# Optimization experiments

Hardware: AMD Instinct MI355X
Metric: run time of the kernel (lower is better)

## Reference

```python
import jax, jax.numpy as jnp
import numpy as np

E = 1024  # embedding_dim
H = 64    # head_size

def setup_inputs() -> dict:
    key = jax.random.key(0)
    k1, k2, k3, k4 = jax.random.split(key, 4)
    x = jax.random.normal(k1, (4, 4096, E), dtype=jnp.float32)
    # nn.Linear(E, H, bias=False) weights have shape [H, E]; y = x @ W.T
    s = 1.0 / np.sqrt(E)
    Wq = jax.random.normal(k2, (H, E), dtype=jnp.float32) * s
    Wk = jax.random.normal(k3, (H, E), dtype=jnp.float32) * s
    Wv = jax.random.normal(k4, (H, E), dtype=jnp.float32) * s
    return {"x": x, "Wq": Wq, "Wk": Wk, "Wv": Wv}

def reference(x, Wq, Wk, Wv):
    B, T, E_ = x.shape
    q = jnp.einsum('bte,he->bth', x, Wq)
    k = jnp.einsum('bte,he->bth', x, Wk)
    v = jnp.einsum('bte,he->bth', x, Wv)
    # NOTE: original scales by sqrt(embedding_dim), not head_size
    scores = jnp.einsum('bqh,bkh->bqk', q, k) / jnp.sqrt(jnp.asarray(E_, x.dtype))
    causal = jnp.tril(jnp.ones((T, T), dtype=bool))
    scores = jnp.where(causal, scores, -jnp.inf)
    weights = jax.nn.softmax(scores, axis=-1)
    return jnp.einsum('bqk,bkh->bqh', weights, v)
```

## Files before the change

### kernel.cpp

```cpp
#include <hip/hip_runtime.h>
#include <stdint.h>

typedef __bf16 bf16x8 __attribute__((ext_vector_type(8)));
typedef float  f32x4  __attribute__((ext_vector_type(4)));

#define E_DIM 1024
#define H_DIM 64
#define T_SEQ 4096
#define B_BAT 4
#define M_TOT (B_BAT * T_SEQ)

__device__ __forceinline__ ushort f2bfu(float f) {
    return __builtin_bit_cast(ushort, (__bf16)f);
}
__device__ __forceinline__ uint32_t pk2(float lo, float hi) {
    return (uint32_t)f2bfu(lo) | ((uint32_t)f2bfu(hi) << 16);
}
__device__ __forceinline__ float ex2(float x) {
    return __builtin_amdgcn_exp2f(x);
}
__device__ __forceinline__ bf16x8 ldfrag(const ushort* p) {
    return __builtin_bit_cast(bf16x8, *(const uint4*)(p));
}
__device__ __forceinline__ void barrier_lgkm() {
    __builtin_amdgcn_s_waitcnt(0xC07F);
    __builtin_amdgcn_s_barrier();
}

__global__ __launch_bounds__(256) void wcvt(const float* __restrict__ Wq,
                                            const float* __restrict__ Wk,
                                            const float* __restrict__ Wv,
                                            ushort* __restrict__ Wfm) {
    int g = blockIdx.x * 256 + threadIdx.x;
    int n = g >> 7;
    int k8 = g & 127;
    const float* src = (n < 64) ? (Wq + (size_t)n * E_DIM)
                     : (n < 128) ? (Wk + (size_t)(n - 64) * E_DIM)
                     : (Wv + (size_t)(n - 128) * E_DIM);
    float sc = (n < 64) ? 0.045084220f : 1.0f;
    float4 a = *(const float4*)(src + k8 * 8);
    float4 b = *(const float4*)(src + k8 * 8 + 4);
    uint4 o;
    o.x = pk2(a.x * sc, a.y * sc); o.y = pk2(a.z * sc, a.w * sc);
    o.z = pk2(b.x * sc, b.y * sc); o.w = pk2(b.z * sc, b.w * sc);
    int s = k8 >> 3, kc = (k8 >> 2) & 1, qd = k8 & 3;
    int nt = n >> 4, lm = n & 15;
    int lane = qd * 16 + lm;
    *(uint4*)(Wfm + (((size_t)(s * 12 + nt) * 2 + kc) * 64 + lane) * 8) = o;
}

__global__ __launch_bounds__(256, 3) void qkv(const float* __restrict__ x,
                                              const ushort* __restrict__ Wfm,
                                              ushort* __restrict__ Qfm,
                                              ushort* __restrict__ Kfm,
                                              ushort* __restrict__ Vfm) {
    __shared__ union {
        ushort a[2][32 * 72];
        struct { ushort c[32 * 136]; ushort vt[64 * 40]; } epi;
    } sm;
    const int tid = threadIdx.x;
    const int w = tid >> 6, l = tid & 63;
    const int lm = l & 15, qd = l >> 4;
    const int m0 = blockIdx.x * 32;

    f32x4 acc[2][3];
#pragma unroll
    for (int r2 = 0; r2 < 2; ++r2)
#pragma unroll
        for (int t = 0; t < 3; ++t) acc[r2][t] = (f32x4){0.f, 0.f, 0.f, 0.f};

    const int srow = tid >> 3, kseg = tid & 7;
    const float* xsrc = x + (size_t)(m0 + srow) * E_DIM + kseg * 8;

    {
        float4 a0 = *(const float4*)xsrc;
        float4 a1 = *(const float4*)(xsrc + 4);
        uint4 u = {pk2(a0.x, a0.y), pk2(a0.z, a0.w), pk2(a1.x, a1.y), pk2(a1.z, a1.w)};
        *(uint4*)(&sm.a[0][srow * 72 + kseg * 8]) = u;
    }
    float4 xa0 = *(const float4*)(xsrc + 64);
    float4 xa1 = *(const float4*)(xsrc + 68);
    float4 xb0 = *(const float4*)(xsrc + 128);
    float4 xb1 = *(const float4*)(xsrc + 132);
    __syncthreads();

    for (int s = 0; s < 16; ++s) {
        const int cb = s & 1, nb = cb ^ 1;
        float4 xc0 = xa0, xc1 = xa1;
        if (s < 13) {
            xc0 = *(const float4*)(xsrc + (s + 3) * 64);
            xc1 = *(const float4*)(xsrc + (s + 3) * 64 + 4);
        }
        bf16x8 wf[3][2];
#pragma unroll
        for (int t = 0; t < 3; ++t)
#pragma unroll
            for (int kc = 0; kc < 2; ++kc)
                wf[t][kc] = ldfrag(Wfm + (((size_t)(s * 12 + w * 3 + t) * 2 + kc) * 64 + l) * 8);
        bf16x8 af[2][2];
#pragma unroll
        for (int r2 = 0; r2 < 2; ++r2)
#pragma unroll
            for (int kc = 0; kc < 2; ++kc)
                af[r2][kc] = ldfrag(&sm.a[cb][(r2 * 16 + lm) * 72 + kc * 32 + qd * 8]);
#pragma unroll
        for (int t = 0; t < 3; ++t)
#pragma unroll
            for (int kc = 0; kc < 2; ++kc)
#pragma unroll
                for (int r2 = 0; r2 < 2; ++r2)
                    acc[r2][t] = __builtin_amdgcn_mfma_f32_16x16x32_bf16(af[r2][kc], wf[t][kc], acc[r2][t], 0, 0, 0);
        if (s < 15) {
            uint4 u = {pk2(xa0.x, xa0.y), pk2(xa0.z, xa0.w), pk2(xa1.x, xa1.y), pk2(xa1.z, xa1.w)};
            *(uint4*)(&sm.a[nb][srow * 72 + kseg * 8]) = u;
        }
        xa0 = xb0; xa1 = xb1; xb0 = xc0; xb1 = xc1;
        if (s < 15) barrier_lgkm();
    }
    __syncthreads();

#pragma unroll
    for (int r2 = 0; r2 < 2; ++r2)
#pragma unroll
        for (int t = 0; t < 3; ++t) {
            int gc = w * 48 + t * 16 + lm;
            int m = r2 * 16 + qd * 4;
#pragma unroll
            for (int rr = 0; rr < 4; ++rr) {
                ushort v = f2bfu(acc[r2][t][rr]);
                if (gc < 128) sm.epi.c[(m + rr) * 136 + gc] = v;
                else          sm.epi.vt[(gc - 128) * 40 + (m + rr)] = v;
            }
        }
    __syncthreads();

    const int g16b = m0 >> 4;
    const int kt64 = m0 >> 6;
    const int tb   = (m0 >> 4) & 3;
    const int kcv  = (m0 >> 5) & 1;
#pragma unroll
    for (int ii = 0; ii < 3; ++ii) {
        int i = w + ii * 4;
        uint4 val;
        ushort* dst;
        if (i < 4) {
            int qt_l = i >> 1, kc = i & 1;
            val = *(const uint4*)(&sm.epi.c[(qt_l * 16 + lm) * 136 + kc * 32 + qd * 8]);
            dst = Qfm + (((size_t)(g16b + qt_l) * 2 + kc) * 64 + l) * 8;
        } else if (i < 8) {
            int j2 = i - 4, t_l = j2 >> 1, kc = j2 & 1;
            val = *(const uint4*)(&sm.epi.c[(t_l * 16 + lm) * 136 + 64 + kc * 32 + qd * 8]);
            dst = Kfm + (((size_t)((kt64 * 4 + tb + t_l) * 2 + kc)) * 64 + l) * 8;
        } else {
            int t = i - 8;
            val = *(const uint4*)(&sm.epi.vt[(t * 16 + lm) * 40 + qd * 8]);
            dst = Vfm + (((size_t)((kt64 * 4 + t) * 2 + kcv)) * 64 + l) * 8;
        }
        *(uint4*)dst = val;
    }
}

__global__ __launch_bounds__(256, 2) void flashm(const ushort* __restrict__ Qfm,
                                                 const ushort* __restrict__ Kfm,
                                                 const ushort* __restrict__ Vfm,
                                                 float* __restrict__ out) {
    __shared__ union {
        ushort plds[4][2][16 * 72];
        struct { float ro[4][16][68]; float rl[4][16]; } red;
    } sm;
    const int tid = threadIdx.x;
    const int wv = tid >> 6, l = tid & 63;
    const int lm = l & 15, qd = l >> 4;
    const int pr = blockIdx.x;
    const int bt = blockIdx.y;
    const int jA = pr, jB = 255 - pr;
    const int ktdA = jA >> 2, tdA = jA & 3;
    const int ktdB = jB >> 2, tdB = jB & 3;
    ushort* mypA = sm.plds[wv][0];
    ushort* mypB = sm.plds[wv][1];

    bf16x8 qA0, qA1, qB0, qB1;
    {
        const ushort* qp = Qfm + ((size_t)(bt * 256 + jA) * 2) * 512 + l * 8;
        qA0 = ldfrag(qp); qA1 = ldfrag(qp + 512);
        const ushort* qq = Qfm + ((size_t)(bt * 256 + jB) * 2) * 512 + l * 8;
        qB0 = ldfrag(qq); qB1 = ldfrag(qq + 512);
    }
    f32x4 oA[4], oB[4];
#pragma unroll
    for (int t = 0; t < 4; ++t) {
        oA[t] = (f32x4){0.f, 0.f, 0.f, 0.f};
        oB[t] = (f32x4){0.f, 0.f, 0.f, 0.f};
    }
    float laccA = 0.f, laccB = 0.f;

    auto emitP = [&](const f32x4* sf, ushort* wp, bool diag, int td, float& lacc) {
#pragma unroll
        for (int t = 0; t < 4; ++t) {
            if (!diag || t < td) {
                float p0 = ex2(sf[t][0]), p1 = ex2(sf[t][1]);
                float p2 = ex2(sf[t][2]), p3 = ex2(sf[t][3]);
                lacc += (p0 + p1) + (p2 + p3);
                *(uint2*)(wp + t * 16) = uint2{pk2(p0, p1), pk2(p2, p3)};
            } else if (t == td) {
                float p[4];
#pragma unroll
                for (int rr = 0; rr < 4; ++rr) {
                    float pe = ex2(sf[t][rr]);
                    if (qd * 4 + rr > lm) pe = 0.f;
                    lacc += pe;
                    p[rr] = pe;
                }
                *(uint2*)(wp + t * 16) = uint2{pk2(p[0], p[1]), pk2(p[2], p[3])};
            } else {
                *(uint2*)(wp + t * 16) = uint2{0u, 0u};
            }
        }
    };
    auto pv = [&](const ushort* myp, const uint4 (&vu)[4][2], f32x4* o) {
        bf16x8 p0 = ldfrag(myp + lm * 72 + qd * 8);
        bf16x8 p1 = ldfrag(myp + lm * 72 + 32 + qd * 8);
#pragma unroll
        for (int t = 0; t < 4; ++t) {
            bf16x8 v0 = __builtin_bit_cast(bf16x8, vu[t][0]);
            bf16x8 v1 = __builtin_bit_cast(bf16x8, vu[t][1]);
            o[t] = __builtin_amdgcn_mfma_f32_16x16x32_bf16(p0, v0, o[t], 0, 0, 0);
            o[t] = __builtin_amdgcn_mfma_f32_16x16x32_bf16(p1, v1, o[t], 0, 0, 0);
        }
    };

    int kt = wv;
#pragma unroll 1
    for (; kt <= ktdA; kt += 4) {
        const ushort* kb = Kfm + ((size_t)(bt * 64 + kt) * 8) * 512;
        const ushort* vb = Vfm + ((size_t)(bt * 64 + kt) * 8) * 512;
        f32x4 sfA[4], sfB[4];
#pragma unroll
        for (int t = 0; t < 4; ++t) {
            sfA[t] = (f32x4){0.f, 0.f, 0.f, 0.f};
            sfB[t] = (f32x4){0.f, 0.f, 0.f, 0.f};
        }
#pragma unroll
        for (int t = 0; t < 4; ++t) {
            bf16x8 k0 = ldfrag(kb + (t * 2 + 0) * 512 + l * 8);
            bf16x8 k1 = ldfrag(kb + (t * 2 + 1) * 512 + l * 8);
            sfB[t] = __builtin_amdgcn_mfma_f32_16x16x32_bf16(k0, qB0, sfB[t], 0, 0, 0);
            sfB[t] = __builtin_amdgcn_mfma_f32_16x16x32_bf16(k1, qB1, sfB[t], 0, 0, 0);
            sfA[t] = __builtin_amdgcn_mfma_f32_16x16x32_bf16(k0, qA0, sfA[t], 0, 0, 0);
            sfA[t] = __builtin_amdgcn_mfma_f32_16x16x32_bf16(k1, qA1, sfA[t], 0, 0, 0);
        }
        uint4 vu[4][2];
#pragma unroll
        for (int t = 0; t < 4; ++t) {
            vu[t][0] = *(const uint4*)(vb + (t * 2 + 0) * 512 + l * 8);
            vu[t][1] = *(const uint4*)(vb + (t * 2 + 1) * 512 + l * 8);
        }
        emitP(sfB, mypB + lm * 72 + qd * 4, false, tdB, laccB);
        emitP(sfA, mypA + lm * 72 + qd * 4, kt == ktdA, tdA, laccA);
        __builtin_amdgcn_wave_barrier();
        __builtin_amdgcn_s_waitcnt(0xC07F);
        __builtin_amdgcn_wave_barrier();
        pv(mypB, vu, oB);
        pv(mypA, vu, oA);
        __builtin_amdgcn_wave_barrier();
    }
#pragma unroll 1
    for (; kt <= ktdB; kt += 4) {
        const ushort* kb = Kfm + ((size_t)(bt * 64 + kt) * 8) * 512;
        const ushort* vb = Vfm + ((size_t)(bt * 64 + kt) * 8) * 512;
        f32x4 sfB[4];
#pragma unroll
        for (int t = 0; t < 4; ++t) sfB[t] = (f32x4){0.f, 0.f, 0.f, 0.f};
#pragma unroll
        for (int t = 0; t < 4; ++t) {
            bf16x8 k0 = ldfrag(kb + (t * 2 + 0) * 512 + l * 8);
            bf16x8 k1 = ldfrag(kb + (t * 2 + 1) * 512 + l * 8);
            sfB[t] = __builtin_amdgcn_mfma_f32_16x16x32_bf16(k0, qB0, sfB[t], 0, 0, 0);
            sfB[t] = __builtin_amdgcn_mfma_f32_16x16x32_bf16(k1, qB1, sfB[t], 0, 0, 0);
        }
        uint4 vu[4][2];
#pragma unroll
        for (int t = 0; t < 4; ++t) {
            vu[t][0] = *(const uint4*)(vb + (t * 2 + 0) * 512 + l * 8);
            vu[t][1] = *(const uint4*)(vb + (t * 2 + 1) * 512 + l * 8);
        }
        emitP(sfB, mypB + lm * 72 + qd * 4, kt == ktdB, tdB, laccB);
        __builtin_amdgcn_wave_barrier();
        __builtin_amdgcn_s_waitcnt(0xC07F);
        __builtin_amdgcn_wave_barrier();
        pv(mypB, vu, oB);
        __builtin_amdgcn_wave_barrier();
    }

    laccA += __shfl_xor(laccA, 16); laccA += __shfl_xor(laccA, 32);
    laccB += __shfl_xor(laccB, 16); laccB += __shfl_xor(laccB, 32);

    __syncthreads();
    if (qd == 0) sm.red.rl[wv][lm] = laccA;
#pragma unroll
    for (int t = 0; t < 4; ++t)
#pragma unroll
        for (int rr = 0; rr < 4; ++rr)
            sm.red.ro[wv][qd * 4 + rr][t * 16 + lm] = oA[t][rr];
    __syncthreads();
    {
        const int row = wv * 4 + qd;
        float ls = sm.red.rl[0][row] + sm.red.rl[1][row] + sm.red.rl[2][row] + sm.red.rl[3][row];
        float inv = 1.0f / ls;
        float4 s0 = *(const float4*)&sm.red.ro[0][row][lm * 4];
        float4 s1 = *(const float4*)&sm.red.ro[1][row][lm * 4];
        float4 s2 = *(const float4*)&sm.red.ro[2][row][lm * 4];
        float4 s3 = *(const float4*)&sm.red.ro[3][row][lm * 4];
        float4 ov;
        ov.x = (s0.x + s1.x + s2.x + s3.x) * inv;
        ov.y = (s0.y + s1.y + s2.y + s3.y) * inv;
        ov.z = (s0.z + s1.z + s2.z + s3.z) * inv;
        ov.w = (s0.w + s1.w + s2.w + s3.w) * inv;
        *(float4*)(out + ((size_t)bt * T_SEQ + jA * 16 + row) * 64 + lm * 4) = ov;
    }
    __syncthreads();
    if (qd == 0) sm.red.rl[wv][lm] = laccB;
#pragma unroll
    for (int t = 0; t < 4; ++t)
#pragma unroll
        for (int rr = 0; rr < 4; ++rr)
            sm.red.ro[wv][qd * 4 + rr][t * 16 + lm] = oB[t][rr];
    __syncthreads();
    {
        const int row = wv * 4 + qd;
        float ls = sm.red.rl[0][row] + sm.red.rl[1][row] + sm.red.rl[2][row] + sm.red.rl[3][row];
        float inv = 1.0f / ls;
        float4 s0 = *(const float4*)&sm.red.ro[0][row][lm * 4];
        float4 s1 = *(const float4*)&sm.red.ro[1][row][lm * 4];
        float4 s2 = *(const float4*)&sm.red.ro[2][row][lm * 4];
        float4 s3 = *(const float4*)&sm.red.ro[3][row][lm * 4];
        float4 ov;
        ov.x = (s0.x + s1.x + s2.x + s3.x) * inv;
        ov.y = (s0.y + s1.y + s2.y + s3.y) * inv;
        ov.z = (s0.z + s1.z + s2.z + s3.z) * inv;
        ov.w = (s0.w + s1.w + s2.w + s3.w) * inv;
        *(float4*)(out + ((size_t)bt * T_SEQ + jB * 16 + row) * 64 + lm * 4) = ov;
    }
}

extern "C" void kernel_launch(void* const* d_in, const int* in_sizes, int n_in,
                              void* d_out, int out_size, void* d_ws, size_t ws_size,
                              hipStream_t stream) {
    const float* x  = (const float*)d_in[0];
    const float* Wq = (const float*)d_in[1];
    const float* Wk = (const float*)d_in[2];
    const float* Wv = (const float*)d_in[3];
    float* out = (float*)d_out;

    char* ws = (char*)d_ws;
    ushort* Wfm = (ushort*)(ws);
    ushort* Qfm = (ushort*)(ws + 393216);
    ushort* Kfm = (ushort*)(ws + 2490368);
    ushort* Vfm = (ushort*)(ws + 4587520);

    wcvt<<<96, 256, 0, stream>>>(Wq, Wk, Wv, Wfm);
    qkv<<<512, 256, 0, stream>>>(x, Wfm, Qfm, Kfm, Vfm);
    flashm<<<dim3(128, B_BAT), 256, 0, stream>>>(Qfm, Kfm, Vfm, out);
}
```

Before: 132.8 us.

## Prefetch next K tile into registers, merge loops, compute row sums via MFMA

Merges the two key-tile loops into one loop with a predicate for the A query tile. The K fragments for the next tile are now loaded into registers during the current iteration, so their latency is hidden behind the QK MFMAs and softmax. The softmax denominators are no longer accumulated with VALU adds and cross-lane shuffles; instead an extra MFMA multiplies P by a vector of ones. The cost is more live registers and an extra pair of MFMAs per tile.

```diff
diff --git a/kernel.cpp b/kernel.cpp
--- a/kernel.cpp
+++ b/kernel.cpp
@@ -179,6 +179,9 @@
     ushort* mypA = sm.plds[wv][0];
     ushort* mypB = sm.plds[wv][1];
 
+    const ushort* kbase = Kfm + ((size_t)(bt * 64) * 8) * 512;
+    const ushort* vbase = Vfm + ((size_t)(bt * 64) * 8) * 512;
+
     bf16x8 qA0, qA1, qB0, qB1;
     {
         const ushort* qp = Qfm + ((size_t)(bt * 256 + jA) * 2) * 512 + l * 8;
@@ -192,15 +195,17 @@
         oA[t] = (f32x4){0.f, 0.f, 0.f, 0.f};
         oB[t] = (f32x4){0.f, 0.f, 0.f, 0.f};
     }
-    float laccA = 0.f, laccB = 0.f;
-
-    auto emitP = [&](const f32x4* sf, ushort* wp, bool diag, int td, float& lacc) {
+    f32x4 lA = (f32x4){0.f, 0.f, 0.f, 0.f};
+    f32x4 lB = (f32x4){0.f, 0.f, 0.f, 0.f};
+    const bf16x8 ones = __builtin_bit_cast(bf16x8,
+        (uint4){0x3F803F80u, 0x3F803F80u, 0x3F803F80u, 0x3F803F80u});
+
+    auto emitP = [&](const f32x4* sf, ushort* wp, bool diag, int td) {
 #pragma unroll
         for (int t = 0; t < 4; ++t) {
             if (!diag || t < td) {
                 float p0 = ex2(sf[t][0]), p1 = ex2(sf[t][1]);
                 float p2 = ex2(sf[t][2]), p3 = ex2(sf[t][3]);
-                lacc += (p0 + p1) + (p2 + p3);
                 *(uint2*)(wp + t * 16) = uint2{pk2(p0, p1), pk2(p2, p3)};
             } else if (t == td) {
                 float p[4];
@@ -208,7 +213,6 @@
                 for (int rr = 0; rr < 4; ++rr) {
                     float pe = ex2(sf[t][rr]);
                     if (qd * 4 + rr > lm) pe = 0.f;
-                    lacc += pe;
                     p[rr] = pe;
                 }
                 *(uint2*)(wp + t * 16) = uint2{pk2(p[0], p[1]), pk2(p[2], p[3])};
@@ -217,7 +221,7 @@
             }
         }
     };
-    auto pv = [&](const ushort* myp, const uint4 (&vu)[4][2], f32x4* o) {
+    auto pv = [&](const ushort* myp, const uint4 (&vu)[4][2], f32x4* o, f32x4& lac) {
         bf16x8 p0 = ldfrag(myp + lm * 72 + qd * 8);
         bf16x8 p1 = ldfrag(myp + lm * 72 + 32 + qd * 8);
 #pragma unroll
@@ -227,13 +231,27 @@
             o[t] = __builtin_amdgcn_mfma_f32_16x16x32_bf16(p0, v0, o[t], 0, 0, 0);
             o[t] = __builtin_amdgcn_mfma_f32_16x16x32_bf16(p1, v1, o[t], 0, 0, 0);
         }
+        lac = __builtin_amdgcn_mfma_f32_16x16x32_bf16(p0, ones, lac, 0, 0, 0);
+        lac = __builtin_amdgcn_mfma_f32_16x16x32_bf16(p1, ones, lac, 0, 0, 0);
     };
 
-    int kt = wv;
+    uint4 ku[8];
+    {
+        const ushort* kb = kbase + (size_t)wv * 8 * 512;
+#pragma unroll
+        for (int i = 0; i < 8; ++i) ku[i] = *(const uint4*)(kb + i * 512 + l * 8);
+    }
+
 #pragma unroll 1
-    for (; kt <= ktdA; kt += 4) {
-        const ushort* kb = Kfm + ((size_t)(bt * 64 + kt) * 8) * 512;
-        const ushort* vb = Vfm + ((size_t)(bt * 64 + kt) * 8) * 512;
+    for (int kt = wv; kt <= ktdB; kt += 4) {
+        const bool actA = (kt <= ktdA);
+        const ushort* vb = vbase + (size_t)kt * 8 * 512;
+        uint4 vu[4][2];
+#pragma unroll
+        for (int t = 0; t < 4; ++t) {
+            vu[t][0] = *(const uint4*)(vb + (t * 2 + 0) * 512 + l * 8);
+            vu[t][1] = *(const uint4*)(vb + (t * 2 + 1) * 512 + l * 8);
+        }
         f32x4 sfA[4], sfB[4];
 #pragma unroll
         for (int t = 0; t < 4; ++t) {
@@ -242,61 +260,35 @@
         }
 #pragma unroll
         for (int t = 0; t < 4; ++t) {
-            bf16x8 k0 = ldfrag(kb + (t * 2 + 0) * 512 + l * 8);
-            bf16x8 k1 = ldfrag(kb + (t * 2 + 1) * 512 + l * 8);
+            bf16x8 k0 = __builtin_bit_cast(bf16x8, ku[t * 2 + 0]);
+            bf16x8 k1 = __builtin_bit_cast(bf16x8, ku[t * 2 + 1]);
             sfB[t] = __builtin_amdgcn_mfma_f32_16x16x32_bf16(k0, qB0, sfB[t], 0, 0, 0);
             sfB[t] = __builtin_amdgcn_mfma_f32_16x16x32_bf16(k1, qB1, sfB[t], 0, 0, 0);
-            sfA[t] = __builtin_amdgcn_mfma_f32_16x16x32_bf16(k0, qA0, sfA[t], 0, 0, 0);
-            sfA[t] = __builtin_amdgcn_mfma_f32_16x16x32_bf16(k1, qA1, sfA[t], 0, 0, 0);
-        }
-        uint4 vu[4][2];
-#pragma unroll
-        for (int t = 0; t < 4; ++t) {
-            vu[t][0] = *(const uint4*)(vb + (t * 2 + 0) * 512 + l * 8);
-            vu[t][1] = *(const uint4*)(vb + (t * 2 + 1) * 512 + l * 8);
-        }
-        emitP(sfB, mypB + lm * 72 + qd * 4, false, tdB, laccB);
-        emitP(sfA, mypA + lm * 72 + qd * 4, kt == ktdA, tdA, laccA);
+            if (actA) {
+                sfA[t] = __builtin_amdgcn_mfma_f32_16x16x32_bf16(k0, qA0, sfA[t], 0, 0, 0);
+                sfA[t] = __builtin_amdgcn_mfma_f32_16x16x32_bf16(k1, qA1, sfA[t], 0, 0, 0);
+            }
+        }
+        if (kt + 4 <= ktdB) {
+            const ushort* kb = kbase + (size_t)(kt + 4) * 8 * 512;
+#pragma unroll
+            for (int i = 0; i < 8; ++i) ku[i] = *(const uint4*)(kb + i * 512 + l * 8);
+        }
+        emitP(sfB, mypB + lm * 72 + qd * 4, kt == ktdB, tdB);
+        if (actA) emitP(sfA, mypA + lm * 72 + qd * 4, kt == ktdA, tdA);
         __builtin_amdgcn_wave_barrier();
         __builtin_amdgcn_s_waitcnt(0xC07F);
         __builtin_amdgcn_wave_barrier();
-        pv(mypB, vu, oB);
-        pv(mypA, vu, oA);
+        pv(mypB, vu, oB, lB);
+        if (actA) pv(mypA, vu, oA, lA);
         __builtin_amdgcn_wave_barrier();
     }
-#pragma unroll 1
-    for (; kt <= ktdB; kt += 4) {
-        const ushort* kb = Kfm + ((size_t)(bt * 64 + kt) * 8) * 512;
-        const ushort* vb = Vfm + ((size_t)(bt * 64 + kt) * 8) * 512;
-        f32x4 sfB[4];
-#pragma unroll
-        for (int t = 0; t < 4; ++t) sfB[t] = (f32x4){0.f, 0.f, 0.f, 0.f};
-#pragma unroll
-        for (int t = 0; t < 4; ++t) {
-            bf16x8 k0 = ldfrag(kb + (t * 2 + 0) * 512 + l * 8);
-            bf16x8 k1 = ldfrag(kb + (t * 2 + 1) * 512 + l * 8);
-            sfB[t] = __builtin_amdgcn_mfma_f32_16x16x32_bf16(k0, qB0, sfB[t], 0, 0, 0);
-            sfB[t] = __builtin_amdgcn_mfma_f32_16x16x32_bf16(k1, qB1, sfB[t], 0, 0, 0);
-        }
-        uint4 vu[4][2];
-#pragma unroll
-        for (int t = 0; t < 4; ++t) {
-            vu[t][0] = *(const uint4*)(vb + (t * 2 + 0) * 512 + l * 8);
-            vu[t][1] = *(const uint4*)(vb + (t * 2 + 1) * 512 + l * 8);
-        }
-        emitP(sfB, mypB + lm * 72 + qd * 4, kt == ktdB, tdB, laccB);
-        __builtin_amdgcn_wave_barrier();
-        __builtin_amdgcn_s_waitcnt(0xC07F);
-        __builtin_amdgcn_wave_barrier();
-        pv(mypB, vu, oB);
-        __builtin_amdgcn_wave_barrier();
-    }
-
-    laccA += __shfl_xor(laccA, 16); laccA += __shfl_xor(laccA, 32);
-    laccB += __shfl_xor(laccB, 16); laccB += __shfl_xor(laccB, 32);
-
-    __syncthreads();
-    if (qd == 0) sm.red.rl[wv][lm] = laccA;
+
+    __syncthreads();
+    if (lm == 0) {
+#pragma unroll
+        for (int rr = 0; rr < 4; ++rr) sm.red.rl[wv][qd * 4 + rr] = lA[rr];
+    }
 #pragma unroll
     for (int t = 0; t < 4; ++t)
 #pragma unroll
@@ -319,7 +311,10 @@
         *(float4*)(out + ((size_t)bt * T_SEQ + jA * 16 + row) * 64 + lm * 4) = ov;
     }
     __syncthreads();
-    if (qd == 0) sm.red.rl[wv][lm] = laccB;
+    if (lm == 0) {
+#pragma unroll
+        for (int rr = 0; rr < 4; ++rr) sm.red.rl[wv][qd * 4 + rr] = lB[rr];
+    }
 #pragma unroll
     for (int t = 0; t < 4; ++t)
 #pragma unroll
```

Result: no change. 131.6 us (-0.9%).
